# Optimization experiments

Measured on AMD Instinct MI355X. Metric: run time of the kernel, lower is better.

The kernel has to match this reference:

```python
import jax, jax.numpy as jnp
import numpy as np

B, T, D, O = 16, 1024, 512, 512

def setup_inputs() -> dict:
    key = jax.random.key(0)
    ks = jax.random.split(key, 16)
    g = lambda k, shape, fan: jax.random.normal(k, shape, jnp.float32) * (1.0 / np.sqrt(fan))
    return {
        "b": jax.random.normal(ks[0], (B, T, D), jnp.float32),
        # attention linears (torch nn.Linear: y = x @ W.T + b), W: [out,in]
        "Wq": g(ks[1], (D, D), D), "bq": jnp.zeros((D,), jnp.float32),
        "Wk": g(ks[2], (D, D), D), "bk": jnp.zeros((D,), jnp.float32),
        "Wv": g(ks[3], (D, D), D), "bv": jnp.zeros((D,), jnp.float32),
        # EMA linears: alpha/delta take concat -> [D, 2D]
        "Wa": g(ks[4], (D, 2 * D), 2 * D), "ba": jnp.zeros((D,), jnp.float32),
        "Wd": g(ks[5], (D, 2 * D), 2 * D), "bd": jnp.zeros((D,), jnp.float32),
        "Wout": g(ks[6], (D, D), D), "bout": jnp.zeros((D,), jnp.float32),
        # MEGADecoder parameters
        "W_f": g(ks[7], (D, D), D), "b_f": jnp.zeros((D,), jnp.float32),
        "W_EMA_c": g(ks[8], (D, D), D),
        "W_z_C": g(ks[9], (D, D), D), "b_C": jnp.zeros((D,), jnp.float32),
        "W_i": g(ks[10], (D, D), D), "b_i": jnp.zeros((D,), jnp.float32),
        "W_o": g(ks[11], (O, D), D), "b_o": jnp.zeros((O,), jnp.float32),
    }

def _forward(b, Wq, bq, Wk, bk, Wv, bv, Wa, ba, Wd, bd, Wout, bout,
             W_f, b_f, W_EMA_c, W_z_C, b_C, W_i, b_i, W_o, b_o):
    batch, t_len, d = b.shape
    # --- EMA recurrence (lax.scan over time) ---
    def step(prev, b_t):  # prev, b_t: [batch, d]
        con = jnp.concatenate([prev, b_t], axis=-1)          # [batch, 2d]
        alpha = jnp.tanh(con @ Wa.T + ba)
        delta = jnp.tanh(con @ Wd.T + bd)
        ema = jax.nn.sigmoid(alpha * b_t + (1.0 - alpha * delta) * prev)
        return ema, ema
    init = jnp.zeros((batch, d), b.dtype)
    _, ema_seq = jax.lax.scan(step, init, jnp.swapaxes(b, 0, 1))  # [t, batch, d]
    ema_seq = jnp.swapaxes(ema_seq, 0, 1)                         # [batch, t, d]
    b_ema = jax.nn.silu(ema_seq @ Wout.T + bout)
    # --- self-attention over b_ema ---
    q = b_ema @ Wq.T + bq
    k = b_ema @ Wk.T + bk
    v = b_ema @ Wv.T + bv
    scores = jnp.einsum('btd,bsd->bts', q, k) / jnp.sqrt(jnp.float32(d))
    attn = jax.nn.softmax(scores, axis=-1)
    Z_EMA = jnp.einsum('bts,bsd->btd', attn, v)
    # --- gated fusion ---
    f = jax.nn.sigmoid(b_ema @ W_f.T + b_f)
    Z_EMA_f = f * Z_EMA
    Z_EMA_C = jax.nn.silu(b_ema @ W_EMA_c + Z_EMA_f @ W_z_C + b_C)
    i = jax.nn.sigmoid(b_ema @ W_i.T + b_i)
    B_h = i * Z_EMA_C + (1.0 - i) * b
    b_cap = B_h @ W_o.T + b_o
    return jax.nn.sigmoid(b_cap)

def reference(b, Wq, bq, Wk, bk, Wv, bv, Wa, ba, Wd, bd, Wout, bout,
              W_f, b_f, W_EMA_c, W_z_C, b_C, W_i, b_i, W_o, b_o):
    return _forward(b, Wq, bq, Wk, bk, Wv, bv, Wa, ba, Wd, bd, Wout, bout,
                    W_f, b_f, W_EMA_c, W_z_C, b_C, W_i, b_i, W_o, b_o)
```

## Files before the change

kernel.cpp:

```cpp
#include <hip/hip_runtime.h>
#include <math.h>

typedef short bf16x8 __attribute__((ext_vector_type(8)));
typedef float f32x4 __attribute__((ext_vector_type(4)));
typedef int   i32x4 __attribute__((ext_vector_type(4)));

#define DEV static __device__ __forceinline__

DEV float bf2f(unsigned short u) {
  union { unsigned int i; float f; } x;
  x.i = ((unsigned int)u) << 16;
  return x.f;
}
DEV unsigned short f2bf(float f) {
  union { float f; unsigned int i; } x;
  x.f = f;
  unsigned int i = x.i;
  i += 0x7fffu + ((i >> 16) & 1u);
  return (unsigned short)(i >> 16);
}
DEV i32x4 load8_cvt(const float* p) {
  const float4 x = *(const float4*)p;
  const float4 y = *(const float4*)(p + 4);
  union { i32x4 v; unsigned short u[8]; } r;
  r.u[0] = f2bf(x.x); r.u[1] = f2bf(x.y); r.u[2] = f2bf(x.z); r.u[3] = f2bf(x.w);
  r.u[4] = f2bf(y.x); r.u[5] = f2bf(y.y); r.u[6] = f2bf(y.z); r.u[7] = f2bf(y.w);
  return r.v;
}
DEV bf16x8 load8_cvt_frag(const float* p) {
  union { i32x4 v; bf16x8 h; } u;
  u.v = load8_cvt(p);
  return u.h;
}

template <int ACT, bool HASBIAS, bool DUALA, bool TRANSC,
          bool AF32, bool BF32, bool CF32>
__global__ __launch_bounds__(256) void gemm_bt(
    const void* __restrict__ A, long long sA, int lda,
    const unsigned short* __restrict__ A2,
    const void* __restrict__ B, long long sB, int ldb,
    const float* __restrict__ bias,
    void* __restrict__ Cout, long long sC,
    int M, int N, int K, float escale)
{
  __shared__ __align__(16) unsigned short Als[128 * 64];
  __shared__ __align__(16) unsigned short Bls[128 * 64];
  const int tid = threadIdx.x;
  const int l = tid & 63;
  const int w = tid >> 6;
  const int wrow = w >> 1, wcol = w & 1;
  const int lane15 = l & 15, quad = l >> 4;
  const long long tm0 = (long long)blockIdx.y * 128;
  const long long tn0 = (long long)blockIdx.x * 128;
  const long long zA = (long long)blockIdx.z * sA;
  const long long zB = (long long)blockIdx.z * sB;
  const float* Af          = (const float*)A;
  const unsigned short* Ah = (const unsigned short*)A;
  const float* Bf          = (const float*)B;
  const unsigned short* Bh = (const unsigned short*)B;

  f32x4 acc[4][4] = {};

  const int srow = tid >> 3;
  const int skb  = tid & 7;
  i32x4 ra[4], rb[4];

  auto gload = [&](int kt) {
    const long long k0 = (long long)kt * 64 + skb * 8;
#pragma unroll
    for (int it = 0; it < 4; ++it) {
      const int r = it * 32 + srow;
      if (DUALA && kt >= 8)
        ra[it] = *(const i32x4*)(A2 + (tm0 + r) * 512 + (k0 - 512));
      else if (AF32)
        ra[it] = load8_cvt(Af + zA + (tm0 + r) * lda + k0);
      else
        ra[it] = *(const i32x4*)(Ah + zA + (tm0 + r) * lda + k0);
      if (BF32)
        rb[it] = load8_cvt(Bf + zB + (tn0 + r) * ldb + k0);
      else
        rb[it] = *(const i32x4*)(Bh + zB + (tn0 + r) * ldb + k0);
    }
  };
  auto swrite = [&]() {
#pragma unroll
    for (int it = 0; it < 4; ++it) {
      const int r = it * 32 + srow;
      const int off = r * 64 + ((skb ^ (r & 7)) * 8);
      *(i32x4*)(Als + off) = ra[it];
      *(i32x4*)(Bls + off) = rb[it];
    }
  };

  gload(0);
  const int NK = K >> 6;
  for (int kt = 0; kt < NK; ++kt) {
    __syncthreads();
    swrite();
    __syncthreads();
    if (kt + 1 < NK) gload(kt + 1);
#pragma unroll
    for (int ks = 0; ks < 2; ++ks) {
      bf16x8 af[4], bfr[4];
#pragma unroll
      for (int ti = 0; ti < 4; ++ti) {
        const int m = wrow * 64 + ti * 16 + lane15;
        const int kb = ks * 4 + quad;
        af[ti] = *(const bf16x8*)(Als + m * 64 + ((kb ^ (m & 7)) * 8));
        const int n = wcol * 64 + ti * 16 + lane15;
        bfr[ti] = *(const bf16x8*)(Bls + n * 64 + ((kb ^ (n & 7)) * 8));
      }
#pragma unroll
      for (int ti = 0; ti < 4; ++ti)
#pragma unroll
        for (int tj = 0; tj < 4; ++tj)
          acc[ti][tj] = __builtin_amdgcn_mfma_f32_16x16x32_bf16(
              af[ti], bfr[tj], acc[ti][tj], 0, 0, 0);
    }
  }

  const long long cb = (long long)blockIdx.z * sC;
#pragma unroll
  for (int tj = 0; tj < 4; ++tj) {
    const long long col = tn0 + wcol * 64 + tj * 16 + lane15;
    const float bvv = HASBIAS ? bias[col] : 0.f;
#pragma unroll
    for (int ti = 0; ti < 4; ++ti) {
#pragma unroll
      for (int r = 0; r < 4; ++r) {
        const long long row = tm0 + wrow * 64 + ti * 16 + quad * 4 + r;
        const long long idx =
            TRANSC ? (((row >> 10) * 512 + col) * 1024 + (row & 1023))
                   : (cb + row * (long long)N + col);
        float v = acc[ti][tj][r] * escale + bvv;
        if (ACT == 1) v = v / (1.f + __expf(-v));
        else if (ACT == 2) v = 1.f / (1.f + __expf(-v));
        if (CF32) ((float*)Cout)[idx] = v;
        else      ((unsigned short*)Cout)[idx] = f2bf(v);
      }
    }
  }
}

__global__ __launch_bounds__(256) void transpose_f2b(
    const float* __restrict__ src, unsigned short* __restrict__ dst,
    int R, int C, int dld)
{
  __shared__ float tile[32][33];
  const int c0 = blockIdx.x * 32, r0 = blockIdx.y * 32;
  const int tx = threadIdx.x & 31, ty = threadIdx.x >> 5;
  for (int i = ty; i < 32; i += 8)
    tile[i][tx] = src[(long long)(r0 + i) * C + c0 + tx];
  __syncthreads();
  for (int i = ty; i < 32; i += 8)
    dst[(long long)(c0 + i) * dld + r0 + tx] = f2bf(tile[tx][i]);
}

__global__ __launch_bounds__(256) void softmax_rows_bf16(
    unsigned short* __restrict__ S)
{
  const long long row = blockIdx.x;
  const int tid = threadIdx.x;
  const ushort4 u = ((const ushort4*)(S + row * 1024))[tid];
  const float a = bf2f(u.x), b = bf2f(u.y), c = bf2f(u.z), d = bf2f(u.w);
  float mx = fmaxf(fmaxf(a, b), fmaxf(c, d));
#pragma unroll
  for (int o = 32; o > 0; o >>= 1) mx = fmaxf(mx, __shfl_xor(mx, o));
  __shared__ float redm[4], reds[4];
  const int w = tid >> 6;
  if ((tid & 63) == 0) redm[w] = mx;
  __syncthreads();
  mx = fmaxf(fmaxf(redm[0], redm[1]), fmaxf(redm[2], redm[3]));
  const float e0 = __expf(a - mx), e1 = __expf(b - mx);
  const float e2 = __expf(c - mx), e3 = __expf(d - mx);
  float s = e0 + e1 + e2 + e3;
#pragma unroll
  for (int o = 32; o > 0; o >>= 1) s += __shfl_xor(s, o);
  if ((tid & 63) == 0) reds[w] = s;
  __syncthreads();
  s = reds[0] + reds[1] + reds[2] + reds[3];
  const float inv = 1.f / s;
  ushort4 o4;
  o4.x = f2bf(e0 * inv); o4.y = f2bf(e1 * inv);
  o4.z = f2bf(e2 * inv); o4.w = f2bf(e3 * inv);
  ((ushort4*)(S + row * 1024))[tid] = o4;
}

__global__ __launch_bounds__(256) void mul_bf16(
    unsigned short* __restrict__ z, const unsigned short* __restrict__ f, int n4)
{
  const int idx = blockIdx.x * 256 + threadIdx.x;
  if (idx >= n4) return;
  ushort4 zv = ((const ushort4*)z)[idx];
  const ushort4 fv = ((const ushort4*)f)[idx];
  zv.x = f2bf(bf2f(zv.x) * bf2f(fv.x));
  zv.y = f2bf(bf2f(zv.y) * bf2f(fv.y));
  zv.z = f2bf(bf2f(zv.z) * bf2f(fv.z));
  zv.w = f2bf(bf2f(zv.w) * bf2f(fv.w));
  ((ushort4*)z)[idx] = zv;
}

__global__ __launch_bounds__(256) void bh_blend(
    const unsigned short* __restrict__ ib, const unsigned short* __restrict__ zc,
    const float* __restrict__ bsrc, unsigned short* __restrict__ out, int n4)
{
  const int idx = blockIdx.x * 256 + threadIdx.x;
  if (idx >= n4) return;
  const ushort4 iv = ((const ushort4*)ib)[idx];
  const ushort4 zv = ((const ushort4*)zc)[idx];
  const float4 bv = ((const float4*)bsrc)[idx];
  ushort4 o;
  const float i0 = bf2f(iv.x), i1 = bf2f(iv.y), i2 = bf2f(iv.z), i3 = bf2f(iv.w);
  o.x = f2bf(i0 * bf2f(zv.x) + (1.f - i0) * bv.x);
  o.y = f2bf(i1 * bf2f(zv.y) + (1.f - i1) * bv.y);
  o.z = f2bf(i2 * bf2f(zv.z) + (1.f - i2) * bv.z);
  o.w = f2bf(i3 * bf2f(zv.w) + (1.f - i3) * bv.w);
  ((ushort4*)out)[idx] = o;
}

__global__ __launch_bounds__(512) void ema_recurrence(
    const float* __restrict__ Wa,
    const float* __restrict__ Wd,
    const unsigned short* __restrict__ Xa,
    const unsigned short* __restrict__ Xd,
    const float* __restrict__ Bin,
    unsigned short* __restrict__ ema,
    unsigned short* __restrict__ prevbuf,
    int* __restrict__ flags)
{
  const int j = blockIdx.x;
  const int tid = threadIdx.x;
  const int l = tid & 63;
  const int w = tid >> 6;
  const int n0 = j * 64;
  const int g = w >> 2;
  const int t4 = w & 3;
  const int lane15 = l & 15;
  const int quad = l >> 4;
  const int ncol = n0 + t4 * 16 + lane15;
  const float* Wsel = g ? Wd : Wa;

  bf16x8 wf[16];
#pragma unroll
  for (int s = 0; s < 16; ++s) {
    const int k = s * 32 + quad * 8;
    wf[s] = load8_cvt_frag(Wsel + (long long)ncol * 1024 + k);
  }

  __shared__ float lds_g[2][16][64];

  const int ei = tid >> 5;
  const int ec = (tid & 31) * 2;
  const int gn = n0 + ec;
  float pv0 = 0.f, pv1 = 0.f;

  for (int t = 0; t < 1024; ++t) {
    const long long eidx = ((long long)ei * 1024 + t) * 512 + gn;
    const unsigned int xau = *(const unsigned int*)(Xa + eidx);
    const unsigned int xdu = *(const unsigned int*)(Xd + eidx);
    const float2 btv = *(const float2*)(Bin + eidx);

    f32x4 acc = {0.f, 0.f, 0.f, 0.f};
    if (t > 0) {
      int guard = 0;
      for (;;) {
        const int fv = __hip_atomic_load(&flags[l & 7], __ATOMIC_RELAXED,
                                         __HIP_MEMORY_SCOPE_AGENT);
        if (__all(fv >= t)) break;
        if (++guard > (1 << 18)) break;
        __builtin_amdgcn_s_sleep(1);
      }
      __builtin_amdgcn_fence(__ATOMIC_ACQUIRE, "agent");

      const unsigned short* pb = prevbuf + ((t - 1) & 1) * (16 * 512);
      bf16x8 af[16];
#pragma unroll
      for (int s = 0; s < 16; ++s) {
        const int k = s * 32 + quad * 8;
        af[s] = *(const bf16x8*)(pb + lane15 * 512 + k);
      }
#pragma unroll
      for (int s = 0; s < 16; ++s)
        acc = __builtin_amdgcn_mfma_f32_16x16x32_bf16(af[s], wf[s], acc, 0, 0, 0);
    }
#pragma unroll
    for (int r = 0; r < 4; ++r)
      lds_g[g][quad * 4 + r][t4 * 16 + lane15] = acc[r];
    __syncthreads();

    float a0 = lds_g[0][ei][ec]     + bf2f((unsigned short)(xau & 0xffffu));
    float a1 = lds_g[0][ei][ec + 1] + bf2f((unsigned short)(xau >> 16));
    float d0 = lds_g[1][ei][ec]     + bf2f((unsigned short)(xdu & 0xffffu));
    float d1 = lds_g[1][ei][ec + 1] + bf2f((unsigned short)(xdu >> 16));
    a0 = tanhf(a0); a1 = tanhf(a1);
    d0 = tanhf(d0); d1 = tanhf(d1);
    const float z0 = a0 * btv.x + (1.f - a0 * d0) * pv0;
    const float z1 = a1 * btv.y + (1.f - a1 * d1) * pv1;
    const float e0 = 1.f / (1.f + __expf(-z0));
    const float e1 = 1.f / (1.f + __expf(-z1));
    pv0 = e0; pv1 = e1;
    const unsigned int packed =
        (unsigned int)f2bf(e0) | ((unsigned int)f2bf(e1) << 16);
    __builtin_nontemporal_store(packed, (unsigned int*)(ema + eidx));
    *(unsigned int*)(prevbuf + (t & 1) * (16 * 512) + (long long)ei * 512 + gn) = packed;
    __syncthreads();
    if (tid == 0)
      __hip_atomic_store(&flags[j], t + 1, __ATOMIC_RELEASE,
                         __HIP_MEMORY_SCOPE_AGENT);
  }
}

extern "C" void kernel_launch(void* const* d_in, const int* in_sizes, int n_in,
                              void* d_out, int out_size, void* d_ws, size_t ws_size,
                              hipStream_t stream)
{
  (void)in_sizes; (void)n_in; (void)out_size; (void)ws_size;
  typedef const float* cfp;
  cfp b     = (cfp)d_in[0];
  cfp Wq    = (cfp)d_in[1];  cfp bq   = (cfp)d_in[2];
  cfp Wk    = (cfp)d_in[3];  cfp bk   = (cfp)d_in[4];
  cfp Wv    = (cfp)d_in[5];  cfp bv   = (cfp)d_in[6];
  cfp Wa    = (cfp)d_in[7];  cfp ba   = (cfp)d_in[8];
  cfp Wd    = (cfp)d_in[9];  cfp bd   = (cfp)d_in[10];
  cfp Wout  = (cfp)d_in[11]; cfp bout = (cfp)d_in[12];
  cfp Wf    = (cfp)d_in[13]; cfp bfb  = (cfp)d_in[14];
  cfp Wemac = (cfp)d_in[15];
  cfp Wzc   = (cfp)d_in[16]; cfp bC   = (cfp)d_in[17];
  cfp Wi    = (cfp)d_in[18]; cfp bi   = (cfp)d_in[19];
  cfp Wo    = (cfp)d_in[20]; cfp bo   = (cfp)d_in[21];

  char* ws = (char*)d_ws;
  const size_t MB = 1024ull * 1024ull;
  typedef unsigned short* bfp;
  bfp S1    = (bfp)(ws + 0);
  bfp S2    = (bfp)(ws + 16 * MB);
  bfp S3    = (bfp)(ws + 32 * MB);
  bfp SC    = (bfp)(ws + 48 * MB);
  bfp W2    = (bfp)(ws + 56 * MB);
  bfp PREV  = (bfp)(ws + 57 * MB);
  int* FLAGS= (int*)(ws + 57 * MB + 64 * 1024);
  bfp OUTH  = (bfp)d_out;

  hipMemsetAsync(FLAGS, 0, 256, stream);

  transpose_f2b<<<dim3(16, 16), 256, 0, stream>>>(Wzc,   W2,       512, 512, 1024);
  transpose_f2b<<<dim3(16, 16), 256, 0, stream>>>(Wemac, W2 + 512, 512, 512, 1024);

  gemm_bt<0, true, false, false, true, true, false><<<dim3(4, 128), 256, 0, stream>>>(
      b, 0, 512, nullptr, Wa + 512, 0, 1024, ba, S1, 0, 16384, 512, 512, 1.f);
  gemm_bt<0, true, false, false, true, true, false><<<dim3(4, 128), 256, 0, stream>>>(
      b, 0, 512, nullptr, Wd + 512, 0, 1024, bd, S2, 0, 16384, 512, 512, 1.f);

  ema_recurrence<<<8, 512, 0, stream>>>(Wa, Wd, S1, S2, b, S3, PREV, FLAGS);

  gemm_bt<1, true, false, false, false, true, false><<<dim3(4, 128), 256, 0, stream>>>(
      S3, 0, 512, nullptr, Wout, 0, 512, bout, S1, 0, 16384, 512, 512, 1.f);

  gemm_bt<0, true, false, false, false, true, false><<<dim3(4, 128), 256, 0, stream>>>(
      S1, 0, 512, nullptr, Wq, 0, 512, bq, S2, 0, 16384, 512, 512, 1.f);
  gemm_bt<0, true, false, false, false, true, false><<<dim3(4, 128), 256, 0, stream>>>(
      S1, 0, 512, nullptr, Wk, 0, 512, bk, S3, 0, 16384, 512, 512, 1.f);
  gemm_bt<0, true, false, true, false, true, false><<<dim3(4, 128), 256, 0, stream>>>(
      S1, 0, 512, nullptr, Wv, 0, 512, bv, OUTH, 0, 16384, 512, 512, 1.f);

  for (int grp = 0; grp < 4; ++grp) {
    const long long go = (long long)grp * 4 * 1024 * 512;
    const long long gv = (long long)grp * 4 * 512 * 1024;
    gemm_bt<0, false, false, false, false, false, false><<<dim3(8, 8, 4), 256, 0, stream>>>(
        S2 + go, 1024 * 512, 512, nullptr, S3 + go, 1024 * 512, 512, nullptr,
        SC, 1024 * 1024, 1024, 1024, 512, 0.04419417382415922f);
    softmax_rows_bf16<<<4096, 256, 0, stream>>>(SC);
    gemm_bt<0, false, false, false, false, false, false><<<dim3(4, 8, 4), 256, 0, stream>>>(
        SC, 1024 * 1024, 1024, nullptr, OUTH + gv, 512 * 1024, 1024, nullptr,
        S2 + go, 1024 * 512, 1024, 512, 1024, 1.f);
  }

  gemm_bt<2, true, false, false, false, true, false><<<dim3(4, 128), 256, 0, stream>>>(
      S1, 0, 512, nullptr, Wf, 0, 512, bfb, S3, 0, 16384, 512, 512, 1.f);

  mul_bf16<<<8192, 256, 0, stream>>>(S2, S3, 2097152);

  gemm_bt<1, true, true, false, false, false, false><<<dim3(4, 128), 256, 0, stream>>>(
      S2, 0, 512, S1, W2, 0, 1024, bC, OUTH, 0, 16384, 512, 1024, 1.f);

  gemm_bt<2, true, false, false, false, true, false><<<dim3(4, 128), 256, 0, stream>>>(
      S1, 0, 512, nullptr, Wi, 0, 512, bi, S3, 0, 16384, 512, 512, 1.f);

  bh_blend<<<8192, 256, 0, stream>>>(S3, OUTH, b, S2, 2097152);

  gemm_bt<2, true, false, false, false, true, true><<<dim3(4, 128), 256, 0, stream>>>(
      S2, 0, 512, nullptr, Wo, 0, 512, bo, d_out, 0, 16384, 512, 512, 1.f);
}
```

Measured before the change: 6.730 ms.

## Split EMA recurrence by batch into independent blocks, drop cross-block flag sync

The recurrence kernel used to split the output columns across 8 blocks that synchronized every timestep through global flags and a global prev buffer. Now 2 blocks of 1024 threads each own 8 batch rows and compute all 512 columns. The previous state lives in swizzled LDS, so the only per-step synchronization is __syncthreads. Each wave holds 4x16 weight fragments in registers and only half the MFMA rows are used, since there are 8 batches per block against 16 MFMA rows. This wastes compute and raises register pressure, and only 2 CUs are used. tanh and sigmoid are replaced with exp-based fast versions.

```diff
diff --git a/kernel.cpp b/kernel.cpp
--- a/kernel.cpp
+++ b/kernel.cpp
@@ -32,6 +32,11 @@
   u.v = load8_cvt(p);
   return u.h;
 }
+DEV float tanh_fast(float x) {
+  const float e = __expf(2.f * x);
+  return 1.f - 2.f / (e + 1.f);
+}
+DEV float sigmoid_fast(float x) { return 1.f / (1.f + __expf(-x)); }
 
 template <int ACT, bool HASBIAS, bool DUALA, bool TRANSC,
           bool AF32, bool BF32, bool CF32>
@@ -218,95 +223,94 @@
   ((ushort4*)out)[idx] = o;
 }
 
-__global__ __launch_bounds__(512) void ema_recurrence(
+__global__ __launch_bounds__(1024, 4) void ema_recurrence(
     const float* __restrict__ Wa,
     const float* __restrict__ Wd,
     const unsigned short* __restrict__ Xa,
     const unsigned short* __restrict__ Xd,
     const float* __restrict__ Bin,
-    unsigned short* __restrict__ ema,
-    unsigned short* __restrict__ prevbuf,
-    int* __restrict__ flags)
-{
-  const int j = blockIdx.x;
+    unsigned short* __restrict__ ema)
+{
+  const int b0 = blockIdx.x * 8;
   const int tid = threadIdx.x;
   const int l = tid & 63;
   const int w = tid >> 6;
-  const int n0 = j * 64;
-  const int g = w >> 2;
-  const int t4 = w & 3;
+  const int g = w >> 3;
+  const int cbk = w & 7;
   const int lane15 = l & 15;
   const int quad = l >> 4;
-  const int ncol = n0 + t4 * 16 + lane15;
   const float* Wsel = g ? Wd : Wa;
 
-  bf16x8 wf[16];
-#pragma unroll
-  for (int s = 0; s < 16; ++s) {
-    const int k = s * 32 + quad * 8;
-    wf[s] = load8_cvt_frag(Wsel + (long long)ncol * 1024 + k);
-  }
-
-  __shared__ float lds_g[2][16][64];
-
-  const int ei = tid >> 5;
-  const int ec = (tid & 31) * 2;
-  const int gn = n0 + ec;
-  float pv0 = 0.f, pv1 = 0.f;
+  bf16x8 wf[4][16];
+#pragma unroll
+  for (int tj = 0; tj < 4; ++tj) {
+    const long long ncol = cbk * 64 + tj * 16 + lane15;
+#pragma unroll
+    for (int s = 0; s < 16; ++s)
+      wf[tj][s] = load8_cvt_frag(Wsel + ncol * 1024 + s * 32 + quad * 8);
+  }
+
+  __shared__ __align__(16) unsigned short lds_prev[16 * 512];
+  __shared__ __align__(16) float lds_g[2][8][512];
+
+  *(i32x4*)(lds_prev + tid * 8) = i32x4{0, 0, 0, 0};
+  __syncthreads();
+
+  const int eb = w >> 1;
+  const int c0 = (w & 1) * 256 + l * 4;
+  const int kb = c0 >> 3;
+  const int pofs = eb * 512 + ((kb ^ (eb & 7)) << 3) + (c0 & 7);
+  float pv0 = 0.f, pv1 = 0.f, pv2 = 0.f, pv3 = 0.f;
+
+  const long long rowbase = (long long)(b0 + eb) * 1024 * 512 + c0;
 
   for (int t = 0; t < 1024; ++t) {
-    const long long eidx = ((long long)ei * 1024 + t) * 512 + gn;
-    const unsigned int xau = *(const unsigned int*)(Xa + eidx);
-    const unsigned int xdu = *(const unsigned int*)(Xd + eidx);
-    const float2 btv = *(const float2*)(Bin + eidx);
-
-    f32x4 acc = {0.f, 0.f, 0.f, 0.f};
+    const long long eidx = rowbase + (long long)t * 512;
+    const ushort4 xa4 = *(const ushort4*)(Xa + eidx);
+    const ushort4 xd4 = *(const ushort4*)(Xd + eidx);
+    const float4  bv4 = *(const float4*)(Bin + eidx);
+
+    f32x4 acc[4] = {};
     if (t > 0) {
-      int guard = 0;
-      for (;;) {
-        const int fv = __hip_atomic_load(&flags[l & 7], __ATOMIC_RELAXED,
-                                         __HIP_MEMORY_SCOPE_AGENT);
-        if (__all(fv >= t)) break;
-        if (++guard > (1 << 18)) break;
-        __builtin_amdgcn_s_sleep(1);
+#pragma unroll
+      for (int s = 0; s < 16; ++s) {
+        const int xk = (s * 4 + quad) ^ (lane15 & 7);
+        const bf16x8 af = *(const bf16x8*)(lds_prev + lane15 * 512 + xk * 8);
+#pragma unroll
+        for (int tj = 0; tj < 4; ++tj)
+          acc[tj] = __builtin_amdgcn_mfma_f32_16x16x32_bf16(
+              af, wf[tj][s], acc[tj], 0, 0, 0);
       }
-      __builtin_amdgcn_fence(__ATOMIC_ACQUIRE, "agent");
-
-      const unsigned short* pb = prevbuf + ((t - 1) & 1) * (16 * 512);
-      bf16x8 af[16];
-#pragma unroll
-      for (int s = 0; s < 16; ++s) {
-        const int k = s * 32 + quad * 8;
-        af[s] = *(const bf16x8*)(pb + lane15 * 512 + k);
-      }
-#pragma unroll
-      for (int s = 0; s < 16; ++s)
-        acc = __builtin_amdgcn_mfma_f32_16x16x32_bf16(af[s], wf[s], acc, 0, 0, 0);
-    }
-#pragma unroll
-    for (int r = 0; r < 4; ++r)
-      lds_g[g][quad * 4 + r][t4 * 16 + lane15] = acc[r];
+    }
+    if (quad < 2) {
+#pragma unroll
+      for (int tj = 0; tj < 4; ++tj)
+#pragma unroll
+        for (int r = 0; r < 4; ++r)
+          lds_g[g][quad * 4 + r][cbk * 64 + tj * 16 + lane15] = acc[tj][r];
+    }
     __syncthreads();
 
-    float a0 = lds_g[0][ei][ec]     + bf2f((unsigned short)(xau & 0xffffu));
-    float a1 = lds_g[0][ei][ec + 1] + bf2f((unsigned short)(xau >> 16));
-    float d0 = lds_g[1][ei][ec]     + bf2f((unsigned short)(xdu & 0xffffu));
-    float d1 = lds_g[1][ei][ec + 1] + bf2f((unsigned short)(xdu >> 16));
-    a0 = tanhf(a0); a1 = tanhf(a1);
-    d0 = tanhf(d0); d1 = tanhf(d1);
-    const float z0 = a0 * btv.x + (1.f - a0 * d0) * pv0;
-    const float z1 = a1 * btv.y + (1.f - a1 * d1) * pv1;
-    const float e0 = 1.f / (1.f + __expf(-z0));
-    const float e1 = 1.f / (1.f + __expf(-z1));
-    pv0 = e0; pv1 = e1;
-    const unsigned int packed =
-        (unsigned int)f2bf(e0) | ((unsigned int)f2bf(e1) << 16);
-    __builtin_nontemporal_store(packed, (unsigned int*)(ema + eidx));
-    *(unsigned int*)(prevbuf + (t & 1) * (16 * 512) + (long long)ei * 512 + gn) = packed;
+    const float4 av = *(const float4*)(&lds_g[0][eb][c0]);
+    const float4 dv = *(const float4*)(&lds_g[1][eb][c0]);
+    const float a0 = tanh_fast(av.x + bf2f(xa4.x));
+    const float a1 = tanh_fast(av.y + bf2f(xa4.y));
+    const float a2 = tanh_fast(av.z + bf2f(xa4.z));
+    const float a3 = tanh_fast(av.w + bf2f(xa4.w));
+    const float d0 = tanh_fast(dv.x + bf2f(xd4.x));
+    const float d1 = tanh_fast(dv.y + bf2f(xd4.y));
+    const float d2 = tanh_fast(dv.z + bf2f(xd4.z));
+    const float d3 = tanh_fast(dv.w + bf2f(xd4.w));
+    const float e0 = sigmoid_fast(a0 * bv4.x + (1.f - a0 * d0) * pv0);
+    const float e1 = sigmoid_fast(a1 * bv4.y + (1.f - a1 * d1) * pv1);
+    const float e2 = sigmoid_fast(a2 * bv4.z + (1.f - a2 * d2) * pv2);
+    const float e3 = sigmoid_fast(a3 * bv4.w + (1.f - a3 * d3) * pv3);
+    pv0 = e0; pv1 = e1; pv2 = e2; pv3 = e3;
+    ushort4 o4;
+    o4.x = f2bf(e0); o4.y = f2bf(e1); o4.z = f2bf(e2); o4.w = f2bf(e3);
+    *(ushort4*)(ema + eidx) = o4;
+    *(ushort4*)(lds_prev + pofs) = o4;
     __syncthreads();
-    if (tid == 0)
-      __hip_atomic_store(&flags[j], t + 1, __ATOMIC_RELEASE,
-                         __HIP_MEMORY_SCOPE_AGENT);
   }
 }
 
@@ -337,11 +341,7 @@
   bfp S3    = (bfp)(ws + 32 * MB);
   bfp SC    = (bfp)(ws + 48 * MB);
   bfp W2    = (bfp)(ws + 56 * MB);
-  bfp PREV  = (bfp)(ws + 57 * MB);
-  int* FLAGS= (int*)(ws + 57 * MB + 64 * 1024);
   bfp OUTH  = (bfp)d_out;
-
-  hipMemsetAsync(FLAGS, 0, 256, stream);
 
   transpose_f2b<<<dim3(16, 16), 256, 0, stream>>>(Wzc,   W2,       512, 512, 1024);
   transpose_f2b<<<dim3(16, 16), 256, 0, stream>>>(Wemac, W2 + 512, 512, 512, 1024);
@@ -351,7 +351,7 @@
   gemm_bt<0, true, false, false, true, true, false><<<dim3(4, 128), 256, 0, stream>>>(
       b, 0, 512, nullptr, Wd + 512, 0, 1024, bd, S2, 0, 16384, 512, 512, 1.f);
 
-  ema_recurrence<<<8, 512, 0, stream>>>(Wa, Wd, S1, S2, b, S3, PREV, FLAGS);
+  ema_recurrence<<<2, 1024, 0, stream>>>(Wa, Wd, S1, S2, b, S3);
 
   gemm_bt<1, true, false, false, false, true, false><<<dim3(4, 128), 256, 0, stream>>>(
       S3, 0, 512, nullptr, Wout, 0, 512, bout, S1, 0, 16384, 512, 512, 1.f);
```

After: 24.89 ms. 270% more time.
